# Kernel optimization log

Measured on AMD Instinct MI355X. Metric: run time of the kernel, lower is better.

The kernel has to match this reference:

```python
import jax, jax.numpy as jnp
import numpy as np

NUM_USER, NUM_ITEM, NUM_TIME = 200000, 100000, 5000
P, Q, R = 32, 32, 32
N = 131072


def _xavier(key, shape):
    fan_in, fan_out = shape[0], int(np.prod(shape[1:]))
    limit = float(np.sqrt(6.0 / (fan_in + fan_out)))
    return jax.random.uniform(key, shape, dtype=jnp.float32, minval=-limit, maxval=limit)


def setup_inputs() -> dict:
    key = jax.random.key(0)
    k1, k2, k3, k4, k5, k6, k7 = jax.random.split(key, 7)
    return {
        "i_input": jax.random.randint(k1, (N,), 0, NUM_USER),
        "j_input": jax.random.randint(k2, (N,), 0, NUM_ITEM),
        "k_input": jax.random.randint(k3, (N,), 0, NUM_TIME),
        "user_embeddings": _xavier(k4, (NUM_USER, P)),
        "item_embeddings": _xavier(k5, (NUM_ITEM, Q)),
        "time_embeddings": _xavier(k6, (NUM_TIME, R)),
        "core_tensor": _xavier(k7, (P, Q, R)),
    }


def reference(i_input, j_input, k_input, user_embeddings, item_embeddings,
              time_embeddings, core_tensor):
    # Gather per-sample embeddings: [n,p], [n,q], [n,r]
    i_embeds = user_embeddings[i_input]
    j_embeds = item_embeddings[j_input]
    k_embeds = time_embeddings[k_input]
    # Fused Tucker contraction: never materialize the (n,p,q,r) outer product.
    # Mathematically identical to einsum('np,nq,nr,pqr->n', ...).
    t = jnp.einsum('np,pqr->nqr', i_embeds, core_tensor)  # [n,q,r]
    t = jnp.einsum('nqr,nq->nr', t, j_embeds)             # [n,r]
    return jnp.einsum('nr,nr->n', t, k_embeds)            # [n]
```

## Files before the change

kernel.cpp:

```cpp
#include <hip/hip_runtime.h>


#define BIN_CAP 128

__global__ __launch_bounds__(256) void scatter_build(
        const int* __restrict__ K, const int* __restrict__ I,
        const int* __restrict__ J, const float* __restrict__ G,
        const float* __restrict__ W, int* __restrict__ counts,
        int4* __restrict__ bins, int* __restrict__ ovf_cnt,
        int4* __restrict__ ovf, float* __restrict__ H,
        int n, int num_time, int n_scatter_blocks) {
    if ((int)blockIdx.x < n_scatter_blocks) {
        const int idx = blockIdx.x * 256 + threadIdx.x;
        if (idx < n) {
            int k = K[idx];
            int4 rec = make_int4(idx, I[idx], J[idx], k);
            int pos = atomicAdd(&counts[k], 1);
            if (pos < BIN_CAP) {
                bins[(size_t)k * BIN_CAP + pos] = rec;
            } else {
                int o = atomicAdd(ovf_cnt, 1);
                ovf[o] = rec;
            }
        }
    } else {
        const int pq4 = threadIdx.x;
        const int kbase = ((int)blockIdx.x - n_scatter_blocks) * 8;

        float acc[8][4];
#pragma unroll
        for (int kk = 0; kk < 8; ++kk)
#pragma unroll
            for (int i = 0; i < 4; ++i) acc[kk][i] = 0.f;

#pragma unroll
        for (int r4 = 0; r4 < 8; ++r4) {
            float4 g[4];
#pragma unroll
            for (int i = 0; i < 4; ++i)
                g[i] = *(const float4*)(G + (size_t)(pq4 * 4 + i) * 32 + r4 * 4);
#pragma unroll
            for (int kk = 0; kk < 8; ++kk) {
                int k = kbase + kk;
                int kc = (k < num_time) ? k : (num_time - 1);
                float4 w = *(const float4*)(W + (size_t)kc * 32 + r4 * 4);
#pragma unroll
                for (int i = 0; i < 4; ++i)
                    acc[kk][i] += g[i].x * w.x + g[i].y * w.y +
                                  g[i].z * w.z + g[i].w * w.w;
            }
        }

#pragma unroll
        for (int kk = 0; kk < 8; ++kk) {
            int k = kbase + kk;
            if (k < num_time) {
                float4 o = make_float4(acc[kk][0], acc[kk][1], acc[kk][2], acc[kk][3]);
                *(float4*)(H + (size_t)k * 1024 + pq4 * 4) = o;
            }
        }
    }
}

__global__ __launch_bounds__(256) void tucker_eval_grouped(
        const float* __restrict__ U, const float* __restrict__ V,
        const float* __restrict__ H, const int* __restrict__ counts,
        const int4* __restrict__ bins, const int* __restrict__ ovf_cnt,
        const int4* __restrict__ ovf, float* __restrict__ out,
        int num_time) {
    __shared__ float4 Hs4[4][256];
    const int wave = threadIdx.x >> 6;
    const int lane = threadIdx.x & 63;
    const int k = blockIdx.x * 4 + wave;
    const int qq = lane & 7;
    const int s8 = lane >> 3;

    int m = 0;
    if (k < num_time) {
        const float4* __restrict__ Hrow4 = (const float4*)(H + (size_t)k * 1024);
#pragma unroll
        for (int c = 0; c < 4; ++c)
            Hs4[wave][lane + 64 * c] = Hrow4[lane + 64 * c];
        m = counts[k];
        m = (m < BIN_CAP) ? m : BIN_CAP;
    }
    __syncthreads();

    if (k < num_time && m > 0) {
        const float4* __restrict__ Hw = Hs4[wave];
        const int4* __restrict__ binsk = bins + (size_t)k * BIN_CAP;
        const int full = m >> 3;

        for (int t = 0; t < full; ++t) {
            const int s = t * 8 + s8;
            int4 rec = binsk[s];
            const float4* __restrict__ Ur = (const float4*)(U + (size_t)rec.y * 32);
            float4 u[8];
#pragma unroll
            for (int p4 = 0; p4 < 8; ++p4) u[p4] = Ur[p4];
            float4 v4 = ((const float4*)(V + (size_t)rec.z * 32))[qq];

            float4 acc = make_float4(0.f, 0.f, 0.f, 0.f);
#pragma unroll
            for (int p4 = 0; p4 < 8; ++p4) {
                float4 h;
                h = Hw[(p4 * 4 + 0) * 8 + qq];
                acc.x += u[p4].x * h.x; acc.y += u[p4].x * h.y;
                acc.z += u[p4].x * h.z; acc.w += u[p4].x * h.w;
                h = Hw[(p4 * 4 + 1) * 8 + qq];
                acc.x += u[p4].y * h.x; acc.y += u[p4].y * h.y;
                acc.z += u[p4].y * h.z; acc.w += u[p4].y * h.w;
                h = Hw[(p4 * 4 + 2) * 8 + qq];
                acc.x += u[p4].z * h.x; acc.y += u[p4].z * h.y;
                acc.z += u[p4].z * h.z; acc.w += u[p4].z * h.w;
                h = Hw[(p4 * 4 + 3) * 8 + qq];
                acc.x += u[p4].w * h.x; acc.y += u[p4].w * h.y;
                acc.z += u[p4].w * h.z; acc.w += u[p4].w * h.w;
            }
            float sd = acc.x * v4.x + acc.y * v4.y + acc.z * v4.z + acc.w * v4.w;
            sd += __shfl_xor(sd, 1, 64);
            sd += __shfl_xor(sd, 2, 64);
            sd += __shfl_xor(sd, 4, 64);
            if (qq == 0) out[rec.x] = sd;
        }

        const int s = full * 8 + s8;
        if (s < m) {
            int4 rec = binsk[s];
            const float4* __restrict__ Ur = (const float4*)(U + (size_t)rec.y * 32);
            float4 u[8];
#pragma unroll
            for (int p4 = 0; p4 < 8; ++p4) u[p4] = Ur[p4];
            float4 v4 = ((const float4*)(V + (size_t)rec.z * 32))[qq];

            float4 acc = make_float4(0.f, 0.f, 0.f, 0.f);
#pragma unroll
            for (int p4 = 0; p4 < 8; ++p4) {
                float4 h;
                h = Hw[(p4 * 4 + 0) * 8 + qq];
                acc.x += u[p4].x * h.x; acc.y += u[p4].x * h.y;
                acc.z += u[p4].x * h.z; acc.w += u[p4].x * h.w;
                h = Hw[(p4 * 4 + 1) * 8 + qq];
                acc.x += u[p4].y * h.x; acc.y += u[p4].y * h.y;
                acc.z += u[p4].y * h.z; acc.w += u[p4].y * h.w;
                h = Hw[(p4 * 4 + 2) * 8 + qq];
                acc.x += u[p4].z * h.x; acc.y += u[p4].z * h.y;
                acc.z += u[p4].z * h.z; acc.w += u[p4].z * h.w;
                h = Hw[(p4 * 4 + 3) * 8 + qq];
                acc.x += u[p4].w * h.x; acc.y += u[p4].w * h.y;
                acc.z += u[p4].w * h.z; acc.w += u[p4].w * h.w;
            }
            float sd = acc.x * v4.x + acc.y * v4.y + acc.z * v4.z + acc.w * v4.w;
            sd += __shfl_xor(sd, 1, 64);
            sd += __shfl_xor(sd, 2, 64);
            sd += __shfl_xor(sd, 4, 64);
            if (qq == 0) out[rec.x] = sd;
        }
    }

    const int cnt = *ovf_cnt;
    if (cnt > 0) {
        const int pg = lane >> 3;
        const int gwave = blockIdx.x * 4 + wave;
        const int nwaves = gridDim.x * 4;
        for (int s = gwave; s < cnt; s += nwaves) {
            int4 rec = ovf[s];
            const float4* __restrict__ Hrow = (const float4*)(H + (size_t)rec.w * 1024);
            const float* __restrict__ Ur = U + (size_t)rec.y * 32;

            float4 acc = make_float4(0.f, 0.f, 0.f, 0.f);
#pragma unroll
            for (int it = 0; it < 4; ++it) {
                float4 h = Hrow[lane + it * 64];
                float up = Ur[pg + it * 8];
                acc.x += up * h.x; acc.y += up * h.y;
                acc.z += up * h.z; acc.w += up * h.w;
            }
#pragma unroll
            for (int off = 8; off < 64; off <<= 1) {
                acc.x += __shfl_xor(acc.x, off, 64);
                acc.y += __shfl_xor(acc.y, off, 64);
                acc.z += __shfl_xor(acc.z, off, 64);
                acc.w += __shfl_xor(acc.w, off, 64);
            }
            float4 v4 = ((const float4*)(V + (size_t)rec.z * 32))[qq];
            float sd = acc.x * v4.x + acc.y * v4.y + acc.z * v4.z + acc.w * v4.w;
            sd += __shfl_xor(sd, 1, 64);
            sd += __shfl_xor(sd, 2, 64);
            sd += __shfl_xor(sd, 4, 64);
            if (lane == 0) out[rec.x] = sd;
        }
    }
}

__global__ __launch_bounds__(256) void build_H(const float* __restrict__ G,
                                               const float* __restrict__ W,
                                               float* __restrict__ H,
                                               int num_time) {
    const int pq4 = threadIdx.x;
    const int kbase = blockIdx.x * 8;
    float acc[8][4];
#pragma unroll
    for (int kk = 0; kk < 8; ++kk)
#pragma unroll
        for (int i = 0; i < 4; ++i) acc[kk][i] = 0.f;
#pragma unroll
    for (int r4 = 0; r4 < 8; ++r4) {
        float4 g[4];
#pragma unroll
        for (int i = 0; i < 4; ++i)
            g[i] = *(const float4*)(G + (size_t)(pq4 * 4 + i) * 32 + r4 * 4);
#pragma unroll
        for (int kk = 0; kk < 8; ++kk) {
            int k = kbase + kk;
            int kc = (k < num_time) ? k : (num_time - 1);
            float4 w = *(const float4*)(W + (size_t)kc * 32 + r4 * 4);
#pragma unroll
            for (int i = 0; i < 4; ++i)
                acc[kk][i] += g[i].x * w.x + g[i].y * w.y + g[i].z * w.z + g[i].w * w.w;
        }
    }
#pragma unroll
    for (int kk = 0; kk < 8; ++kk) {
        int k = kbase + kk;
        if (k < num_time) {
            float4 o = make_float4(acc[kk][0], acc[kk][1], acc[kk][2], acc[kk][3]);
            *(float4*)(H + (size_t)k * 1024 + pq4 * 4) = o;
        }
    }
}

__global__ __launch_bounds__(256) void tucker_eval(const int* __restrict__ I,
                                                   const int* __restrict__ J,
                                                   const int* __restrict__ K,
                                                   const float* __restrict__ U,
                                                   const float* __restrict__ V,
                                                   const float* __restrict__ H,
                                                   float* __restrict__ out,
                                                   int n_samples) {
    const int wave = (int)((blockIdx.x * (unsigned)blockDim.x + threadIdx.x) >> 6);
    const int lane = threadIdx.x & 63;
    if (wave >= n_samples) return;
    const int i = I[wave];
    const int j = J[wave];
    const int k = K[wave];
    const int qq = lane & 7;
    const int pg = lane >> 3;
    const float4* __restrict__ Hrow = (const float4*)(H + (size_t)k * 1024);
    const float* __restrict__ Urow = U + (size_t)i * 32;
    float4 acc = make_float4(0.f, 0.f, 0.f, 0.f);
#pragma unroll
    for (int it = 0; it < 4; ++it) {
        float4 h = Hrow[lane + it * 64];
        float up = Urow[pg + it * 8];
        acc.x += up * h.x; acc.y += up * h.y;
        acc.z += up * h.z; acc.w += up * h.w;
    }
#pragma unroll
    for (int off = 8; off < 64; off <<= 1) {
        acc.x += __shfl_xor(acc.x, off, 64);
        acc.y += __shfl_xor(acc.y, off, 64);
        acc.z += __shfl_xor(acc.z, off, 64);
        acc.w += __shfl_xor(acc.w, off, 64);
    }
    float4 v4 = ((const float4*)(V + (size_t)j * 32))[qq];
    float s = acc.x * v4.x + acc.y * v4.y + acc.z * v4.z + acc.w * v4.w;
    s += __shfl_xor(s, 1, 64);
    s += __shfl_xor(s, 2, 64);
    s += __shfl_xor(s, 4, 64);
    if (lane == 0) out[wave] = s;
}

__global__ __launch_bounds__(256) void tucker_direct(const int* __restrict__ I,
                                                     const int* __restrict__ J,
                                                     const int* __restrict__ K,
                                                     const float* __restrict__ U,
                                                     const float* __restrict__ V,
                                                     const float* __restrict__ W,
                                                     const float* __restrict__ G,
                                                     float* __restrict__ out,
                                                     int n_samples) {
    __shared__ float Gc[4 * 32 * 32];
    const int n = blockIdx.x * blockDim.x + threadIdx.x;
    const bool active = (n < n_samples);
    int i = 0, j = 0, k = 0;
    if (active) { i = I[n]; j = J[n]; k = K[n]; }
    float4 w4[8];
#pragma unroll
    for (int r4 = 0; r4 < 8; ++r4)
        w4[r4] = ((const float4*)(W + (size_t)k * 32))[r4];
    float v[32];
#pragma unroll
    for (int q4 = 0; q4 < 8; ++q4) {
        float4 t = ((const float4*)(V + (size_t)j * 32))[q4];
        v[q4 * 4 + 0] = t.x; v[q4 * 4 + 1] = t.y;
        v[q4 * 4 + 2] = t.z; v[q4 * 4 + 3] = t.w;
    }
    const float* __restrict__ Urow = U + (size_t)i * 32;
    float acc = 0.f;
    for (int c = 0; c < 8; ++c) {
        __syncthreads();
#pragma unroll
        for (int t = 0; t < 4; ++t) {
            int idx = threadIdx.x + t * 256;
            ((float4*)Gc)[idx] = ((const float4*)(G + (size_t)c * 4096))[idx];
        }
        __syncthreads();
        for (int pp = 0; pp < 4; ++pp) {
            float up = Urow[c * 4 + pp];
#pragma unroll
            for (int q = 0; q < 32; ++q) {
                float t0 = 0.f;
#pragma unroll
                for (int r4 = 0; r4 < 8; ++r4) {
                    float4 g = ((const float4*)Gc)[pp * 256 + q * 8 + r4];
                    t0 += g.x * w4[r4].x + g.y * w4[r4].y + g.z * w4[r4].z + g.w * w4[r4].w;
                }
                acc += up * v[q] * t0;
            }
        }
    }
    if (active) out[n] = acc;
}

extern "C" void kernel_launch(void* const* d_in, const int* in_sizes, int n_in,
                              void* d_out, int out_size, void* d_ws, size_t ws_size,
                              hipStream_t stream) {
    const int*   I = (const int*)d_in[0];
    const int*   J = (const int*)d_in[1];
    const int*   K = (const int*)d_in[2];
    const float* U = (const float*)d_in[3];
    const float* V = (const float*)d_in[4];
    const float* W = (const float*)d_in[5];
    const float* G = (const float*)d_in[6];
    float* out = (float*)d_out;

    const int n_samples = in_sizes[0];
    const int num_time = in_sizes[5] / 32;

    const size_t h_bytes = (size_t)num_time * 1024 * sizeof(float);
    const size_t z_bytes = (size_t)(num_time + 1) * sizeof(int);
    const size_t z_pad = (z_bytes + 15) & ~(size_t)15;
    const size_t bins_bytes = (size_t)num_time * BIN_CAP * sizeof(int4);
    const size_t ovf_bytes = (size_t)n_samples * sizeof(int4);
    const size_t need_full = h_bytes + z_pad + bins_bytes + ovf_bytes;

    if (ws_size >= need_full) {
        float* H       = (float*)d_ws;
        int*   counts  = (int*)((char*)d_ws + h_bytes);
        int*   ovf_cnt = counts + num_time;
        int4*  bins    = (int4*)((char*)d_ws + h_bytes + z_pad);
        int4*  ovf     = (int4*)((char*)d_ws + h_bytes + z_pad + bins_bytes);

        const int sb = (n_samples + 255) / 256;
        const int bb = (num_time + 7) / 8;

        hipMemsetAsync(counts, 0, z_bytes, stream);
        scatter_build<<<sb + bb, 256, 0, stream>>>(K, I, J, G, W, counts, bins,
                                                   ovf_cnt, ovf, H, n_samples,
                                                   num_time, sb);
        tucker_eval_grouped<<<(num_time + 3) / 4, 256, 0, stream>>>(
            U, V, H, counts, bins, ovf_cnt, ovf, out, num_time);
    } else if (ws_size >= h_bytes) {
        float* H = (float*)d_ws;
        build_H<<<(num_time + 7) / 8, 256, 0, stream>>>(G, W, H, num_time);
        const long long total_threads = (long long)n_samples * 64;
        tucker_eval<<<(int)((total_threads + 255) / 256), 256, 0, stream>>>(
            I, J, K, U, V, H, out, n_samples);
    } else {
        tucker_direct<<<(n_samples + 255) / 256, 256, 0, stream>>>(
            I, J, K, U, V, W, G, out, n_samples);
    }
}
```

Before: 137.1 us.

## Fuse memset, scatter, H build and eval into one cooperative kernel

Measured after the change: 137.2 us. No clear change (+0.0%).

```diff
diff --git a/kernel.cpp b/kernel.cpp
--- a/kernel.cpp
+++ b/kernel.cpp
@@ -1,7 +1,199 @@
 #include <hip/hip_runtime.h>
+#include <hip/hip_cooperative_groups.h>
+
+namespace cg = cooperative_groups;
 
 
 #define BIN_CAP 128
+
+__global__ __launch_bounds__(256, 5) void tucker_fused(
+        const int* __restrict__ K, const int* __restrict__ I,
+        const int* __restrict__ J, const float* __restrict__ G,
+        const float* __restrict__ W, const float* __restrict__ U,
+        const float* __restrict__ V, int* __restrict__ counts,
+        int4* __restrict__ bins, int* __restrict__ ovf_cnt,
+        int4* __restrict__ ovf, float* __restrict__ out,
+        int n, int num_time) {
+    cg::grid_group grid = cg::this_grid();
+    const int gtid = blockIdx.x * 256 + (int)threadIdx.x;
+    const int gsize = gridDim.x * 256;
+
+    for (int c = gtid; c < num_time + 1; c += gsize) counts[c] = 0;
+    grid.sync();
+
+    for (int idx = gtid; idx < n; idx += gsize) {
+        int k = K[idx];
+        int4 rec = make_int4(idx, I[idx], J[idx], k);
+        int pos = atomicAdd(&counts[k], 1);
+        if (pos < BIN_CAP) {
+            bins[(size_t)k * BIN_CAP + pos] = rec;
+        } else {
+            int o = atomicAdd(ovf_cnt, 1);
+            ovf[o] = rec;
+        }
+    }
+    grid.sync();
+
+    __shared__ float4 Hs4[4][256];
+    const int kbase = blockIdx.x * 4;
+
+    {
+        const int t = threadIdx.x;
+        float acc[4][4];
+#pragma unroll
+        for (int kk = 0; kk < 4; ++kk)
+#pragma unroll
+            for (int i = 0; i < 4; ++i) acc[kk][i] = 0.f;
+
+#pragma unroll
+        for (int r4 = 0; r4 < 8; ++r4) {
+            float4 g[4];
+#pragma unroll
+            for (int i = 0; i < 4; ++i)
+                g[i] = *(const float4*)(G + (size_t)(t * 4 + i) * 32 + r4 * 4);
+#pragma unroll
+            for (int kk = 0; kk < 4; ++kk) {
+                int k = kbase + kk;
+                int kc = (k < num_time) ? k : (num_time - 1);
+                float4 w = *(const float4*)(W + (size_t)kc * 32 + r4 * 4);
+#pragma unroll
+                for (int i = 0; i < 4; ++i)
+                    acc[kk][i] += g[i].x * w.x + g[i].y * w.y +
+                                  g[i].z * w.z + g[i].w * w.w;
+            }
+        }
+#pragma unroll
+        for (int kk = 0; kk < 4; ++kk)
+            Hs4[kk][t] = make_float4(acc[kk][0], acc[kk][1], acc[kk][2], acc[kk][3]);
+    }
+    __syncthreads();
+
+    const int wave = threadIdx.x >> 6;
+    const int lane = threadIdx.x & 63;
+    const int k = kbase + wave;
+    const int qq = lane & 7;
+    const int s8 = lane >> 3;
+
+    if (k < num_time) {
+        int m = counts[k];
+        m = (m < BIN_CAP) ? m : BIN_CAP;
+        if (m > 0) {
+            const float4* __restrict__ Hw = Hs4[wave];
+            const int4* __restrict__ binsk = bins + (size_t)k * BIN_CAP;
+            const int full = m >> 3;
+
+            for (int t = 0; t < full; ++t) {
+                const int s = t * 8 + s8;
+                int4 rec = binsk[s];
+                const float4* __restrict__ Ur = (const float4*)(U + (size_t)rec.y * 32);
+                float4 u[8];
+#pragma unroll
+                for (int p4 = 0; p4 < 8; ++p4) u[p4] = Ur[p4];
+                float4 v4 = ((const float4*)(V + (size_t)rec.z * 32))[qq];
+
+                float4 acc = make_float4(0.f, 0.f, 0.f, 0.f);
+#pragma unroll
+                for (int p4 = 0; p4 < 8; ++p4) {
+                    float4 h;
+                    h = Hw[(p4 * 4 + 0) * 8 + qq];
+                    acc.x += u[p4].x * h.x; acc.y += u[p4].x * h.y;
+                    acc.z += u[p4].x * h.z; acc.w += u[p4].x * h.w;
+                    h = Hw[(p4 * 4 + 1) * 8 + qq];
+                    acc.x += u[p4].y * h.x; acc.y += u[p4].y * h.y;
+                    acc.z += u[p4].y * h.z; acc.w += u[p4].y * h.w;
+                    h = Hw[(p4 * 4 + 2) * 8 + qq];
+                    acc.x += u[p4].z * h.x; acc.y += u[p4].z * h.y;
+                    acc.z += u[p4].z * h.z; acc.w += u[p4].z * h.w;
+                    h = Hw[(p4 * 4 + 3) * 8 + qq];
+                    acc.x += u[p4].w * h.x; acc.y += u[p4].w * h.y;
+                    acc.z += u[p4].w * h.z; acc.w += u[p4].w * h.w;
+                }
+                float sd = acc.x * v4.x + acc.y * v4.y + acc.z * v4.z + acc.w * v4.w;
+                sd += __shfl_xor(sd, 1, 64);
+                sd += __shfl_xor(sd, 2, 64);
+                sd += __shfl_xor(sd, 4, 64);
+                if (qq == 0) out[rec.x] = sd;
+            }
+
+            const int s = full * 8 + s8;
+            if (s < m) {
+                int4 rec = binsk[s];
+                const float4* __restrict__ Ur = (const float4*)(U + (size_t)rec.y * 32);
+                float4 u[8];
+#pragma unroll
+                for (int p4 = 0; p4 < 8; ++p4) u[p4] = Ur[p4];
+                float4 v4 = ((const float4*)(V + (size_t)rec.z * 32))[qq];
+
+                float4 acc = make_float4(0.f, 0.f, 0.f, 0.f);
+#pragma unroll
+                for (int p4 = 0; p4 < 8; ++p4) {
+                    float4 h;
+                    h = Hw[(p4 * 4 + 0) * 8 + qq];
+                    acc.x += u[p4].x * h.x; acc.y += u[p4].x * h.y;
+                    acc.z += u[p4].x * h.z; acc.w += u[p4].x * h.w;
+                    h = Hw[(p4 * 4 + 1) * 8 + qq];
+                    acc.x += u[p4].y * h.x; acc.y += u[p4].y * h.y;
+                    acc.z += u[p4].y * h.z; acc.w += u[p4].y * h.w;
+                    h = Hw[(p4 * 4 + 2) * 8 + qq];
+                    acc.x += u[p4].z * h.x; acc.y += u[p4].z * h.y;
+                    acc.z += u[p4].z * h.z; acc.w += u[p4].z * h.w;
+                    h = Hw[(p4 * 4 + 3) * 8 + qq];
+                    acc.x += u[p4].w * h.x; acc.y += u[p4].w * h.y;
+                    acc.z += u[p4].w * h.z; acc.w += u[p4].w * h.w;
+                }
+                float sd = acc.x * v4.x + acc.y * v4.y + acc.z * v4.z + acc.w * v4.w;
+                sd += __shfl_xor(sd, 1, 64);
+                sd += __shfl_xor(sd, 2, 64);
+                sd += __shfl_xor(sd, 4, 64);
+                if (qq == 0) out[rec.x] = sd;
+            }
+        }
+    }
+
+    const int cnt = *ovf_cnt;
+    if (cnt > 0) {
+        const int pg = lane >> 3;
+        const int gwave = blockIdx.x * 4 + wave;
+        const int nwaves = gridDim.x * 4;
+        for (int s = gwave; s < cnt; s += nwaves) {
+            int4 rec = ovf[s];
+            const float* __restrict__ Ur = U + (size_t)rec.y * 32;
+            const float4* __restrict__ Wr = (const float4*)(W + (size_t)rec.w * 32);
+
+            float4 acc = make_float4(0.f, 0.f, 0.f, 0.f);
+#pragma unroll
+            for (int it = 0; it < 4; ++it) {
+                const int p = it * 8 + pg;
+                float hc[4] = {0.f, 0.f, 0.f, 0.f};
+                for (int r4 = 0; r4 < 8; ++r4) {
+                    float4 w = Wr[r4];
+#pragma unroll
+                    for (int c = 0; c < 4; ++c) {
+                        float4 g = *(const float4*)(
+                            G + (size_t)(p * 32 + qq * 4 + c) * 32 + r4 * 4);
+                        hc[c] += g.x * w.x + g.y * w.y + g.z * w.z + g.w * w.w;
+                    }
+                }
+                float up = Ur[p];
+                acc.x += up * hc[0]; acc.y += up * hc[1];
+                acc.z += up * hc[2]; acc.w += up * hc[3];
+            }
+#pragma unroll
+            for (int off = 8; off < 64; off <<= 1) {
+                acc.x += __shfl_xor(acc.x, off, 64);
+                acc.y += __shfl_xor(acc.y, off, 64);
+                acc.z += __shfl_xor(acc.z, off, 64);
+                acc.w += __shfl_xor(acc.w, off, 64);
+            }
+            float4 v4 = ((const float4*)(V + (size_t)rec.z * 32))[qq];
+            float sd = acc.x * v4.x + acc.y * v4.y + acc.z * v4.z + acc.w * v4.w;
+            sd += __shfl_xor(sd, 1, 64);
+            sd += __shfl_xor(sd, 2, 64);
+            sd += __shfl_xor(sd, 4, 64);
+            if (lane == 0) out[rec.x] = sd;
+        }
+    }
+}
 
 __global__ __launch_bounds__(256) void scatter_build(
         const int* __restrict__ K, const int* __restrict__ I,
@@ -26,13 +218,11 @@
     } else {
         const int pq4 = threadIdx.x;
         const int kbase = ((int)blockIdx.x - n_scatter_blocks) * 8;
-
         float acc[8][4];
 #pragma unroll
         for (int kk = 0; kk < 8; ++kk)
 #pragma unroll
             for (int i = 0; i < 4; ++i) acc[kk][i] = 0.f;
-
 #pragma unroll
         for (int r4 = 0; r4 < 8; ++r4) {
             float4 g[4];
@@ -50,7 +240,6 @@
                                   g[i].z * w.z + g[i].w * w.w;
             }
         }
-
 #pragma unroll
         for (int kk = 0; kk < 8; ++kk) {
             int k = kbase + kk;
@@ -99,7 +288,6 @@
 #pragma unroll
             for (int p4 = 0; p4 < 8; ++p4) u[p4] = Ur[p4];
             float4 v4 = ((const float4*)(V + (size_t)rec.z * 32))[qq];
-
             float4 acc = make_float4(0.f, 0.f, 0.f, 0.f);
 #pragma unroll
             for (int p4 = 0; p4 < 8; ++p4) {
@@ -123,7 +311,6 @@
             sd += __shfl_xor(sd, 4, 64);
             if (qq == 0) out[rec.x] = sd;
         }
-
         const int s = full * 8 + s8;
         if (s < m) {
             int4 rec = binsk[s];
@@ -132,7 +319,6 @@
 #pragma unroll
             for (int p4 = 0; p4 < 8; ++p4) u[p4] = Ur[p4];
             float4 v4 = ((const float4*)(V + (size_t)rec.z * 32))[qq];
-
             float4 acc = make_float4(0.f, 0.f, 0.f, 0.f);
 #pragma unroll
             for (int p4 = 0; p4 < 8; ++p4) {
@@ -167,7 +353,6 @@
             int4 rec = ovf[s];
             const float4* __restrict__ Hrow = (const float4*)(H + (size_t)rec.w * 1024);
             const float* __restrict__ Ur = U + (size_t)rec.y * 32;
-
             float4 acc = make_float4(0.f, 0.f, 0.f, 0.f);
 #pragma unroll
             for (int it = 0; it < 4; ++it) {
@@ -352,14 +537,46 @@
         int4*  bins    = (int4*)((char*)d_ws + h_bytes + z_pad);
         int4*  ovf     = (int4*)((char*)d_ws + h_bytes + z_pad + bins_bytes);
 
+        const int grid_blocks = (num_time + 3) / 4;
+
+        int dev = 0;
+        (void)hipGetDevice(&dev);
+        int coop = 0;
+        (void)hipDeviceGetAttribute(&coop, hipDeviceAttributeCooperativeLaunch, dev);
+        int num_cu = 0;
+        (void)hipDeviceGetAttribute(&num_cu, hipDeviceAttributeMultiprocessorCount, dev);
+        int max_blocks_per_cu = 0;
+        (void)hipOccupancyMaxActiveBlocksPerMultiprocessor(
+            &max_blocks_per_cu, (const void*)tucker_fused, 256, 0);
+
+        bool use_coop = (coop != 0) &&
+                        ((long long)max_blocks_per_cu * num_cu >= grid_blocks);
+
+        if (use_coop) {
+            const int*   Ka = K;  const int* Ia = I;  const int* Ja = J;
+            const float* Ga = G;  const float* Wa = W;
+            const float* Ua = U;  const float* Va = V;
+            int*  countsa = counts;  int4* binsa = bins;
+            int*  ovfca = ovf_cnt;   int4* ovfa = ovf;
+            float* outa = out;
+            int na = n_samples, nta = num_time;
+            void* kargs[] = {
+                (void*)&Ka, (void*)&Ia, (void*)&Ja, (void*)&Ga, (void*)&Wa,
+                (void*)&Ua, (void*)&Va, (void*)&countsa, (void*)&binsa,
+                (void*)&ovfca, (void*)&ovfa, (void*)&outa, (void*)&na, (void*)&nta};
+            hipError_t e = hipLaunchCooperativeKernel(
+                (const void*)tucker_fused, dim3(grid_blocks), dim3(256),
+                kargs, 0, stream);
+            if (e == hipSuccess) return;
+        }
+
         const int sb = (n_samples + 255) / 256;
         const int bb = (num_time + 7) / 8;
-
         hipMemsetAsync(counts, 0, z_bytes, stream);
         scatter_build<<<sb + bb, 256, 0, stream>>>(K, I, J, G, W, counts, bins,
                                                    ovf_cnt, ovf, H, n_samples,
                                                    num_time, sb);
-        tucker_eval_grouped<<<(num_time + 3) / 4, 256, 0, stream>>>(
+        tucker_eval_grouped<<<grid_blocks, 256, 0, stream>>>(
             U, V, H, counts, bins, ovf_cnt, ovf, out, num_time);
     } else if (ws_size >= h_bytes) {
         float* H = (float*)d_ws;
```
